# Performance work log

Measured on AMD Instinct MI355X. Metric: run time of the kernel, lower is better.

The kernel has to match this reference:

```python
import jax, jax.numpy as jnp
import numpy as np
from jax import lax

B, T, E, H, VC, VP = 128, 512, 256, 512, 64, 128


def _uniform(key, shape, bound):
    return jax.random.uniform(key, shape, minval=-bound, maxval=bound, dtype=jnp.float32)


def setup_inputs() -> dict:
    key = jax.random.key(0)
    ks = jax.random.split(key, 12)
    src = jax.random.randint(ks[0], (B, T), 0, VC)
    src_lengths = jax.random.randint(ks[1], (B,), 1, T + 1)
    # embedding table, padding_idx=0 row zeroed (as nn.Embedding does)
    emb_table = jax.random.normal(ks[2], (VC, E), dtype=jnp.float32)
    emb_table = emb_table.at[0].set(0.0)
    # layer 0: W_xh Linear(E->H, bias), W_hh Linear(H->H, no bias)
    bE, bH = 1.0 / np.sqrt(E), 1.0 / np.sqrt(H)
    W_xh0 = _uniform(ks[3], (E, H), bE)
    b_xh0 = _uniform(ks[4], (H,), bE)
    W_hh0 = _uniform(ks[5], (H, H), bH)
    # layer 1: input is hidden of layer 0
    W_xh1 = _uniform(ks[6], (H, H), bH)
    b_xh1 = _uniform(ks[7], (H,), bH)
    W_hh1 = _uniform(ks[8], (H, H), bH)
    # output projection Linear(H -> VP)
    fc_w = _uniform(ks[9], (H, VP), bH)
    fc_b = _uniform(ks[10], (VP,), bH)
    return {
        "src": src, "src_lengths": src_lengths, "emb_table": emb_table,
        "W_xh0": W_xh0, "b_xh0": b_xh0, "W_hh0": W_hh0,
        "W_xh1": W_xh1, "b_xh1": b_xh1, "W_hh1": W_hh1,
        "fc_w": fc_w, "fc_b": fc_b,
    }


def reference(src, src_lengths, emb_table, W_xh0, b_xh0, W_hh0,
              W_xh1, b_xh1, W_hh1, fc_w, fc_b):
    batch, seq_len = src.shape
    emb = emb_table[src]  # (B, T, E); dropout p=0 -> identity (eval)
    mask = jnp.arange(seq_len)[None, :] < src_lengths[:, None]  # (B, T) bool

    xs = jnp.transpose(emb, (1, 0, 2))          # (T, B, E) time-major
    ms = jnp.transpose(mask)[:, :, None]        # (T, B, 1)

    def step(h, inp):
        x_t, m_t = inp
        h0, h1 = h
        h0_new = jnp.tanh(x_t @ W_xh0 + b_xh0 + h0 @ W_hh0)
        h0 = jnp.where(m_t, h0_new, h0)
        h1_new = jnp.tanh(h0 @ W_xh1 + b_xh1 + h1 @ W_hh1)
        h1 = jnp.where(m_t, h1_new, h1)
        return (h0, h1), h1

    h_init = jnp.zeros((batch, W_hh0.shape[0]), dtype=emb.dtype)
    _, ys = lax.scan(step, (h_init, h_init), (xs, ms))  # ys: (T, B, H)
    outputs = jnp.transpose(ys, (1, 0, 2))               # (B, T, H)
    logits = outputs @ fc_w + fc_b                       # (B, T, VP)
    return logits
```

## Files before the change

kernel.cpp:

```cpp
#include <hip/hip_runtime.h>
#include <hip/hip_bf16.h>

constexpr int NB = 128;
constexpr int NT = 512;
constexpr int NE = 256;
constexpr int NH = 512;
constexpr int NV = 64;
constexpr int NP = 128;

constexpr int GROUPS = 8;
constexpr int MR     = 16;
constexpr int NCS    = 64;
constexpr int SLICES = 8;
constexpr int NBLK   = GROUPS * SLICES * 2;
constexpr int RING   = 16;
constexpr int FS     = 32;

typedef unsigned short u16;
typedef __attribute__((ext_vector_type(8))) short bf16x8v;
typedef __attribute__((ext_vector_type(4))) float f32x4v;
typedef __attribute__((ext_vector_type(4))) unsigned u32x4;

__device__ __forceinline__ u16 f2bf(float x) {
  unsigned u = __builtin_bit_cast(unsigned, x);
  return (u16)((u + 0x7fffu + ((u >> 16) & 1u)) >> 16);
}

__device__ __forceinline__ void ld4_sc1(const void* p0, const void* p1,
                                        const void* p2, const void* p3,
                                        u32x4& a, u32x4& b, u32x4& c, u32x4& d) {
  asm volatile("global_load_dwordx4 %0, %4, off sc1\n\t"
               "global_load_dwordx4 %1, %5, off sc1\n\t"
               "global_load_dwordx4 %2, %6, off sc1\n\t"
               "global_load_dwordx4 %3, %7, off sc1\n\t"
               "s_waitcnt vmcnt(0)"
               : "=&v"(a), "=&v"(b), "=&v"(c), "=&v"(d)
               : "v"(p0), "v"(p1), "v"(p2), "v"(p3) : "memory");
}
__device__ __forceinline__ void ld8_sc1(const void* p0, const void* p1,
                                        const void* p2, const void* p3,
                                        const void* p4, const void* p5,
                                        const void* p6, const void* p7,
                                        u32x4& a, u32x4& b, u32x4& c, u32x4& d,
                                        u32x4& e, u32x4& f, u32x4& g, u32x4& h) {
  asm volatile("global_load_dwordx4 %0, %8, off sc1\n\t"
               "global_load_dwordx4 %1, %9, off sc1\n\t"
               "global_load_dwordx4 %2, %10, off sc1\n\t"
               "global_load_dwordx4 %3, %11, off sc1\n\t"
               "global_load_dwordx4 %4, %12, off sc1\n\t"
               "global_load_dwordx4 %5, %13, off sc1\n\t"
               "global_load_dwordx4 %6, %14, off sc1\n\t"
               "global_load_dwordx4 %7, %15, off sc1\n\t"
               "s_waitcnt vmcnt(0)"
               : "=&v"(a), "=&v"(b), "=&v"(c), "=&v"(d),
                 "=&v"(e), "=&v"(f), "=&v"(g), "=&v"(h)
               : "v"(p0), "v"(p1), "v"(p2), "v"(p3),
                 "v"(p4), "v"(p5), "v"(p6), "v"(p7) : "memory");
}
__device__ __forceinline__ void st_sc1_x4(void* p, u32x4 v) {
  asm volatile("global_store_dwordx4 %0, %1, off sc1" :: "v"(p), "v"(v) : "memory");
}

__global__ __launch_bounds__(256) void proj_kernel(
    const float* __restrict__ emb, const float* __restrict__ W_xh0,
    const float* __restrict__ b_xh0, float* __restrict__ proj) {
  int v = blockIdx.x >> 1;
  int j = ((blockIdx.x & 1) << 8) + threadIdx.x;
  float acc = b_xh0[j];
  const float* er = emb + v * NE;
  for (int e = 0; e < NE; ++e) acc += er[e] * W_xh0[e * NH + j];
  proj[v * NH + j] = acc;
}

__global__ __launch_bounds__(256) void transpose_bf16_kernel(
    const float* __restrict__ src, u16* __restrict__ dst, int R, int logC) {
  int idx = blockIdx.x * 256 + threadIdx.x;
  int C = 1 << logC;
  if (idx >= R * C) return;
  int r = idx >> logC;
  int c = idx & (C - 1);
  dst[c * R + r] = f2bf(src[idx]);
}

__global__ void zero_flags_kernel(int* flags) {
  int i = blockIdx.x * 256 + threadIdx.x;
  if (i < 2 * 64 * FS) flags[i] = 0;
}

__device__ __forceinline__ bf16x8v frag_A(const u16* __restrict__ buf,
                                          int kt, int lane) {
  return *(const bf16x8v*)(buf + (kt << 9) + (((lane ^ kt) & 63) << 3));
}

__device__ __forceinline__ void publish_slice(const u16* __restrict__ rep,
                                              u16* __restrict__ gpanel,
                                              int sl, int tid) {
  if (tid < 128) {
    int ktl = tid >> 6, slot = tid & 63;
    int ktp = sl * 2 + ktl;
    int v = (slot ^ ktp) & 63;
    int row = v & 15, koct = (v >> 4) & 3;
    int lcol = ktl * 32 + koct * 8;
    st_sc1_x4(gpanel + ktp * 512 + slot * 8,
              *(const u32x4*)(rep + row * 64 + lcol));
  }
}

__global__ __launch_bounds__(256, 1) void rnn_persist(
    const int* __restrict__ src, const int* __restrict__ lens,
    const float* __restrict__ proj,
    const u16* __restrict__ Wt_hh0,
    const u16* __restrict__ Wt_xh1,
    const u16* __restrict__ Wt_hh1,
    const float* __restrict__ b_xh1,
    u16* __restrict__ h0f,
    u16* __restrict__ h1f,
    int* __restrict__ flags)
{
  __shared__ struct {
    union {
      struct { __attribute__((aligned(16))) u16 a0[8192];
               float pj[NV][68]; int srcv[MR][NT]; } l0;
      struct { __attribute__((aligned(16))) u16 a0[8192];
               __attribute__((aligned(16))) u16 a1[8192]; } l1;
    } u;
    __attribute__((aligned(16))) u16 rep[16][64];
  } sm;

  const int bid = blockIdx.x;
  const bool is_l1 = (bid >= 64);
  const int rb = bid & 63;
  const int g = rb & (GROUPS - 1);
  const int sl = rb >> 3;
  const int c0 = sl * NCS;
  const int r0 = g * MR;

  const int tid = threadIdx.x;
  const int lane = tid & 63, wave = tid >> 6;
  const int lq = lane >> 4, lr = lane & 15;
  const int lcol = wave * 16 + lr;

  int* flag0 = flags;
  int* flag1 = flags + 64 * FS;
  int* myflag = (is_l1 ? flag1 : flag0) + rb * FS;

  int ln[4];
#pragma unroll
  for (int i = 0; i < 4; ++i) ln[i] = lens[r0 + lq * 4 + i];
  u16 oreg[4] = {0, 0, 0, 0};

  if (!is_l1) {
    bf16x8v w0[16];
    {
      const u16* wp = Wt_hh0 + (size_t)(c0 + lcol) * NH + lq * 8;
#pragma unroll
      for (int kt = 0; kt < 16; ++kt) w0[kt] = *(const bf16x8v*)(wp + kt * 32);
    }
#pragma unroll
    for (int it = 0; it < 4; ++it) {
      int c = it * 256 + tid;
      int v = c >> 4, j4 = (c & 15) * 4;
      *(float4*)&sm.u.l0.pj[v][j4] = *(const float4*)&proj[v * NH + c0 + j4];
    }
#pragma unroll
    for (int it = 0; it < 8; ++it)
      ((int4*)sm.u.l0.srcv)[it * 256 + tid] =
          ((const int4*)(src + (size_t)r0 * NT))[it * 256 + tid];
    __syncthreads();

    for (int s = 0; s < NT; ++s) {
      f32x4v acc = {0.f, 0.f, 0.f, 0.f};
      if (s > 0) {
        if (tid < 8) {
          const int* fp = flag0 + ((tid * 8) | g) * FS;
          while (__hip_atomic_load(fp, __ATOMIC_RELAXED,
                                   __HIP_MEMORY_SCOPE_AGENT) < s) {}
        } else if (tid < 16 && s - 14 > 0) {
          const int* fp = flag1 + (((tid - 8) * 8) | g) * FS;
          while (__hip_atomic_load(fp, __ATOMIC_RELAXED,
                                   __HIP_MEMORY_SCOPE_AGENT) < s - 14) {}
        }
        if (tid < 64) __builtin_amdgcn_fence(__ATOMIC_ACQUIRE, "agent");
        __syncthreads();
        {
          const u16* gp = h0f + ((size_t)((s - 1) & (RING - 1)) * GROUPS + g) * 8192;
          u32x4 a, b, c, d;
          ld4_sc1(gp + (tid + 0) * 8, gp + (tid + 256) * 8,
                  gp + (tid + 512) * 8, gp + (tid + 768) * 8, a, b, c, d);
          *(u32x4*)(sm.u.l0.a0 + (tid + 0) * 8) = a;
          *(u32x4*)(sm.u.l0.a0 + (tid + 256) * 8) = b;
          *(u32x4*)(sm.u.l0.a0 + (tid + 512) * 8) = c;
          *(u32x4*)(sm.u.l0.a0 + (tid + 768) * 8) = d;
        }
        __syncthreads();
#pragma unroll
        for (int kt = 0; kt < 16; ++kt)
          acc = __builtin_amdgcn_mfma_f32_16x16x32_bf16(
              frag_A(sm.u.l0.a0, kt, lane), w0[kt], acc, 0, 0, 0);
      }
#pragma unroll
      for (int i = 0; i < 4; ++i) {
        int row = lq * 4 + i;
        float pre = acc[i] + sm.u.l0.pj[sm.u.l0.srcv[row][s]][lcol];
        oreg[i] = (s < ln[i]) ? f2bf(tanhf(pre)) : oreg[i];
        sm.rep[row][lcol] = oreg[i];
      }
      __syncthreads();
      publish_slice(&sm.rep[0][0],
                    h0f + ((size_t)(s & (RING - 1)) * GROUPS + g) * 8192, sl, tid);
      asm volatile("s_waitcnt vmcnt(0)" ::: "memory");
      __syncthreads();
      if (tid == 0)
        __hip_atomic_store(myflag, s + 1, __ATOMIC_RELAXED,
                           __HIP_MEMORY_SCOPE_AGENT);
    }
  } else {
    bf16x8v wx[16], wh[16];
    {
      const u16* wpx = Wt_xh1 + (size_t)(c0 + lcol) * NH + lq * 8;
      const u16* wph = Wt_hh1 + (size_t)(c0 + lcol) * NH + lq * 8;
#pragma unroll
      for (int kt = 0; kt < 16; ++kt) {
        wx[kt] = *(const bf16x8v*)(wpx + kt * 32);
        wh[kt] = *(const bf16x8v*)(wph + kt * 32);
      }
    }
    const float bcol = b_xh1[c0 + lcol];
    __syncthreads();

    for (int t = 0; t < NT; ++t) {
      if (tid < 8) {
        if (t > 0) {
          const int* fp = flag1 + ((tid * 8) | g) * FS;
          while (__hip_atomic_load(fp, __ATOMIC_RELAXED,
                                   __HIP_MEMORY_SCOPE_AGENT) < t) {}
        }
      } else if (tid < 16) {
        const int* fp = flag0 + (((tid - 8) * 8) | g) * FS;
        while (__hip_atomic_load(fp, __ATOMIC_RELAXED,
                                 __HIP_MEMORY_SCOPE_AGENT) < t + 1) {}
      }
      if (tid < 64) __builtin_amdgcn_fence(__ATOMIC_ACQUIRE, "agent");
      __syncthreads();
      {
        const u16* g0 = h0f + ((size_t)(t & (RING - 1)) * GROUPS + g) * 8192;
        if (t > 0) {
          const u16* g1 = h1f + ((size_t)(t - 1) * GROUPS + g) * 8192;
          u32x4 a, b, c, d, e, f, h, k;
          ld8_sc1(g0 + (tid + 0) * 8, g0 + (tid + 256) * 8,
                  g0 + (tid + 512) * 8, g0 + (tid + 768) * 8,
                  g1 + (tid + 0) * 8, g1 + (tid + 256) * 8,
                  g1 + (tid + 512) * 8, g1 + (tid + 768) * 8,
                  a, b, c, d, e, f, h, k);
          *(u32x4*)(sm.u.l1.a0 + (tid + 0) * 8) = a;
          *(u32x4*)(sm.u.l1.a0 + (tid + 256) * 8) = b;
          *(u32x4*)(sm.u.l1.a0 + (tid + 512) * 8) = c;
          *(u32x4*)(sm.u.l1.a0 + (tid + 768) * 8) = d;
          *(u32x4*)(sm.u.l1.a1 + (tid + 0) * 8) = e;
          *(u32x4*)(sm.u.l1.a1 + (tid + 256) * 8) = f;
          *(u32x4*)(sm.u.l1.a1 + (tid + 512) * 8) = h;
          *(u32x4*)(sm.u.l1.a1 + (tid + 768) * 8) = k;
        } else {
          u32x4 a, b, c, d;
          ld4_sc1(g0 + (tid + 0) * 8, g0 + (tid + 256) * 8,
                  g0 + (tid + 512) * 8, g0 + (tid + 768) * 8, a, b, c, d);
          *(u32x4*)(sm.u.l1.a0 + (tid + 0) * 8) = a;
          *(u32x4*)(sm.u.l1.a0 + (tid + 256) * 8) = b;
          *(u32x4*)(sm.u.l1.a0 + (tid + 512) * 8) = c;
          *(u32x4*)(sm.u.l1.a0 + (tid + 768) * 8) = d;
        }
      }
      __syncthreads();

      f32x4v accx = {0.f, 0.f, 0.f, 0.f}, acch = {0.f, 0.f, 0.f, 0.f};
#pragma unroll
      for (int kt = 0; kt < 16; ++kt)
        accx = __builtin_amdgcn_mfma_f32_16x16x32_bf16(
            frag_A(sm.u.l1.a0, kt, lane), wx[kt], accx, 0, 0, 0);
      if (t > 0) {
#pragma unroll
        for (int kt = 0; kt < 16; ++kt)
          acch = __builtin_amdgcn_mfma_f32_16x16x32_bf16(
              frag_A(sm.u.l1.a1, kt, lane), wh[kt], acch, 0, 0, 0);
      }
#pragma unroll
      for (int i = 0; i < 4; ++i) {
        int row = lq * 4 + i;
        float pre = accx[i] + acch[i] + bcol;
        oreg[i] = (t < ln[i]) ? f2bf(tanhf(pre)) : oreg[i];
        sm.rep[row][lcol] = oreg[i];
      }
      __syncthreads();
      publish_slice(&sm.rep[0][0],
                    h1f + ((size_t)t * GROUPS + g) * 8192, sl, tid);
      asm volatile("s_waitcnt vmcnt(0)" ::: "memory");
      __syncthreads();
      if (tid == 0)
        __hip_atomic_store(myflag, t + 1, __ATOMIC_RELAXED,
                           __HIP_MEMORY_SCOPE_AGENT);
    }
  }
}

__global__ __launch_bounds__(256) void out_gemm(
    const u16* __restrict__ h1f, const u16* __restrict__ fc_wT,
    const float* __restrict__ fc_b, float* __restrict__ out)
{
  const int t = blockIdx.x;
  const int tid = threadIdx.x, lane = tid & 63, wave = tid >> 6;
  const int lq = lane >> 4, lr = lane & 15;
  const int m0 = wave * 32;
  f32x4v acc[2][8];
#pragma unroll
  for (int a = 0; a < 2; ++a)
#pragma unroll
    for (int b = 0; b < 8; ++b) acc[a][b] = (f32x4v){0.f, 0.f, 0.f, 0.f};

  const u16* p0 = h1f + ((size_t)t * GROUPS + wave * 2) * 8192;
  const u16* p1 = p0 + 8192;
#pragma unroll 2
  for (int kt = 0; kt < 16; ++kt) {
    bf16x8v a0 = *(const bf16x8v*)(p0 + kt * 512 + (((lane ^ kt) & 63) << 3));
    bf16x8v a1 = *(const bf16x8v*)(p1 + kt * 512 + (((lane ^ kt) & 63) << 3));
    int kb = kt * 32 + lq * 8;
#pragma unroll
    for (int ni = 0; ni < 8; ++ni) {
      bf16x8v bb = *(const bf16x8v*)(fc_wT + (size_t)(ni * 16 + lr) * NH + kb);
      acc[0][ni] = __builtin_amdgcn_mfma_f32_16x16x32_bf16(a0, bb, acc[0][ni], 0, 0, 0);
      acc[1][ni] = __builtin_amdgcn_mfma_f32_16x16x32_bf16(a1, bb, acc[1][ni], 0, 0, 0);
    }
  }
#pragma unroll
  for (int mi = 0; mi < 2; ++mi)
#pragma unroll
    for (int ni = 0; ni < 8; ++ni)
#pragma unroll
      for (int i = 0; i < 4; ++i) {
        int b_ = m0 + mi * 16 + lq * 4 + i;
        int p = ni * 16 + lr;
        out[((size_t)b_ * NT + t) * NP + p] = acc[mi][ni][i] + fc_b[p];
      }
}

extern "C" void kernel_launch(void* const* d_in, const int* in_sizes, int n_in,
                              void* d_out, int out_size, void* d_ws, size_t ws_size,
                              hipStream_t stream) {
  const int*   src   = (const int*)  d_in[0];
  const int*   lens  = (const int*)  d_in[1];
  const float* emb   = (const float*)d_in[2];
  const float* W_xh0 = (const float*)d_in[3];
  const float* b_xh0 = (const float*)d_in[4];
  const float* W_hh0 = (const float*)d_in[5];
  const float* W_xh1 = (const float*)d_in[6];
  const float* b_xh1 = (const float*)d_in[7];
  const float* W_hh1 = (const float*)d_in[8];
  const float* fc_w  = (const float*)d_in[9];
  const float* fc_b  = (const float*)d_in[10];
  float* out = (float*)d_out;

  char* ws = (char*)d_ws;
  auto alloc = [&](size_t bytes) { char* p = ws; ws += (bytes + 255) & ~size_t(255); return p; };
  float* proj   = (float*)alloc(NV * NH * 4);
  u16* Wt_hh0   = (u16*)  alloc(NH * NH * 2);
  u16* Wt_xh1   = (u16*)  alloc(NH * NH * 2);
  u16* Wt_hh1   = (u16*)  alloc(NH * NH * 2);
  u16* fc_wT    = (u16*)  alloc(NP * NH * 2);
  u16* h0f      = (u16*)  alloc((size_t)RING * GROUPS * 8192 * 2);
  u16* h1f      = (u16*)  alloc((size_t)NT * GROUPS * 8192 * 2);
  int* flags    = (int*)  alloc(2 * 64 * FS * 4);

  proj_kernel<<<NV * 2, 256, 0, stream>>>(emb, W_xh0, b_xh0, proj);
  transpose_bf16_kernel<<<(NH * NH + 255) / 256, 256, 0, stream>>>(W_hh0, Wt_hh0, NH, 9);
  transpose_bf16_kernel<<<(NH * NH + 255) / 256, 256, 0, stream>>>(W_xh1, Wt_xh1, NH, 9);
  transpose_bf16_kernel<<<(NH * NH + 255) / 256, 256, 0, stream>>>(W_hh1, Wt_hh1, NH, 9);
  transpose_bf16_kernel<<<(NH * NP + 255) / 256, 256, 0, stream>>>(fc_w, fc_wT, NH, 7);
  zero_flags_kernel<<<(2 * 64 * FS + 255) / 256, 256, 0, stream>>>(flags);

  {
    void* kargs[] = { (void*)&src, (void*)&lens, (void*)&proj, (void*)&Wt_hh0,
                      (void*)&Wt_xh1, (void*)&Wt_hh1, (void*)&b_xh1,
                      (void*)&h0f, (void*)&h1f, (void*)&flags };
    hipError_t e = hipLaunchCooperativeKernel((void*)rnn_persist, dim3(NBLK), dim3(256),
                                              kargs, 0, stream);
    if (e != hipSuccess) {
      rnn_persist<<<NBLK, 256, 0, stream>>>(src, lens, proj, Wt_hh0, Wt_xh1,
                                            Wt_hh1, b_xh1, h0f, h1f, flags);
    }
  }

  out_gemm<<<NT, 256, 0, stream>>>(h1f, fc_wT, fc_b, out);
}
```

Measured before the change: 1.547 ms.

## Overlap flag publish with peer-flag polling across waves and drop a barrier

```diff
diff --git a/kernel.cpp b/kernel.cpp
--- a/kernel.cpp
+++ b/kernel.cpp
@@ -92,17 +92,19 @@
   return *(const bf16x8v*)(buf + (kt << 9) + (((lane ^ kt) & 63) << 3));
 }
 
-__device__ __forceinline__ void publish_slice(const u16* __restrict__ rep,
-                                              u16* __restrict__ gpanel,
-                                              int sl, int tid) {
-  if (tid < 128) {
-    int ktl = tid >> 6, slot = tid & 63;
+__device__ __forceinline__ void publish_w0(const u16* __restrict__ rep,
+                                           u16* __restrict__ gpanel,
+                                           int sl, int lane) {
+#pragma unroll
+  for (int hh = 0; hh < 2; ++hh) {
+    int c = hh * 64 + lane;
+    int ktl = c >> 6, slot = c & 63;
     int ktp = sl * 2 + ktl;
     int v = (slot ^ ktp) & 63;
     int row = v & 15, koct = (v >> 4) & 3;
-    int lcol = ktl * 32 + koct * 8;
+    int lc = ktl * 32 + koct * 8;
     st_sc1_x4(gpanel + ktp * 512 + slot * 8,
-              *(const u32x4*)(rep + row * 64 + lcol));
+              *(const u32x4*)(rep + row * 64 + lc));
   }
 }
 
@@ -171,15 +173,6 @@
     for (int s = 0; s < NT; ++s) {
       f32x4v acc = {0.f, 0.f, 0.f, 0.f};
       if (s > 0) {
-        if (tid < 8) {
-          const int* fp = flag0 + ((tid * 8) | g) * FS;
-          while (__hip_atomic_load(fp, __ATOMIC_RELAXED,
-                                   __HIP_MEMORY_SCOPE_AGENT) < s) {}
-        } else if (tid < 16 && s - 14 > 0) {
-          const int* fp = flag1 + (((tid - 8) * 8) | g) * FS;
-          while (__hip_atomic_load(fp, __ATOMIC_RELAXED,
-                                   __HIP_MEMORY_SCOPE_AGENT) < s - 14) {}
-        }
         if (tid < 64) __builtin_amdgcn_fence(__ATOMIC_ACQUIRE, "agent");
         __syncthreads();
         {
@@ -206,13 +199,28 @@
         sm.rep[row][lcol] = oreg[i];
       }
       __syncthreads();
-      publish_slice(&sm.rep[0][0],
-                    h0f + ((size_t)(s & (RING - 1)) * GROUPS + g) * 8192, sl, tid);
-      asm volatile("s_waitcnt vmcnt(0)" ::: "memory");
-      __syncthreads();
-      if (tid == 0)
-        __hip_atomic_store(myflag, s + 1, __ATOMIC_RELAXED,
-                           __HIP_MEMORY_SCOPE_AGENT);
+      if (wave == 0) {
+        publish_w0(&sm.rep[0][0],
+                   h0f + ((size_t)(s & (RING - 1)) * GROUPS + g) * 8192, sl, lane);
+        asm volatile("s_waitcnt vmcnt(0)" ::: "memory");
+        if (lane == 0)
+          __hip_atomic_store(myflag, s + 1, __ATOMIC_RELAXED,
+                             __HIP_MEMORY_SCOPE_AGENT);
+      } else if (wave == 2) {
+        if (s + 1 < NT && lane < 8 && lane != sl) {
+          const int* fp = flag0 + ((lane << 3) | g) * FS;
+          while (__hip_atomic_load(fp, __ATOMIC_RELAXED,
+                                   __HIP_MEMORY_SCOPE_AGENT) < s + 1) {}
+        }
+      } else if (wave == 3) {
+        int need = s + 1 - 14;
+        if (s + 1 < NT && lane < 8 && need > 0) {
+          const int* fp = flag1 + ((lane << 3) | g) * FS;
+          while (__hip_atomic_load(fp, __ATOMIC_RELAXED,
+                                   __HIP_MEMORY_SCOPE_AGENT) < need) {}
+        }
+      }
+      __syncthreads();
     }
   } else {
     bf16x8v wx[16], wh[16];
@@ -227,19 +235,14 @@
     }
     const float bcol = b_xh1[c0 + lcol];
     __syncthreads();
+    if (tid < 8) {
+      const int* fp = flag0 + ((tid << 3) | g) * FS;
+      while (__hip_atomic_load(fp, __ATOMIC_RELAXED,
+                               __HIP_MEMORY_SCOPE_AGENT) < 1) {}
+    }
+    __syncthreads();
 
     for (int t = 0; t < NT; ++t) {
-      if (tid < 8) {
-        if (t > 0) {
-          const int* fp = flag1 + ((tid * 8) | g) * FS;
-          while (__hip_atomic_load(fp, __ATOMIC_RELAXED,
-                                   __HIP_MEMORY_SCOPE_AGENT) < t) {}
-        }
-      } else if (tid < 16) {
-        const int* fp = flag0 + (((tid - 8) * 8) | g) * FS;
-        while (__hip_atomic_load(fp, __ATOMIC_RELAXED,
-                                 __HIP_MEMORY_SCOPE_AGENT) < t + 1) {}
-      }
       if (tid < 64) __builtin_amdgcn_fence(__ATOMIC_ACQUIRE, "agent");
       __syncthreads();
       {
@@ -291,13 +294,27 @@
         sm.rep[row][lcol] = oreg[i];
       }
       __syncthreads();
-      publish_slice(&sm.rep[0][0],
-                    h1f + ((size_t)t * GROUPS + g) * 8192, sl, tid);
-      asm volatile("s_waitcnt vmcnt(0)" ::: "memory");
-      __syncthreads();
-      if (tid == 0)
-        __hip_atomic_store(myflag, t + 1, __ATOMIC_RELAXED,
-                           __HIP_MEMORY_SCOPE_AGENT);
+      if (wave == 0) {
+        publish_w0(&sm.rep[0][0],
+                   h1f + ((size_t)t * GROUPS + g) * 8192, sl, lane);
+        asm volatile("s_waitcnt vmcnt(0)" ::: "memory");
+        if (lane == 0)
+          __hip_atomic_store(myflag, t + 1, __ATOMIC_RELAXED,
+                             __HIP_MEMORY_SCOPE_AGENT);
+      } else if (wave == 2) {
+        if (t + 1 < NT && lane < 8 && lane != sl) {
+          const int* fp = flag1 + ((lane << 3) | g) * FS;
+          while (__hip_atomic_load(fp, __ATOMIC_RELAXED,
+                                   __HIP_MEMORY_SCOPE_AGENT) < t + 1) {}
+        }
+      } else if (wave == 3) {
+        if (t + 1 < NT && lane < 8) {
+          const int* fp = flag0 + ((lane << 3) | g) * FS;
+          while (__hip_atomic_load(fp, __ATOMIC_RELAXED,
+                                   __HIP_MEMORY_SCOPE_AGENT) < t + 2) {}
+        }
+      }
+      __syncthreads();
     }
   }
 }
```

New measurement: 1.697 ms. 1.1x slower.

## Repartition persistent RNN onto fewer, wider blocks with 512 threads

Applied to the files above, without the earlier changes.

```diff
diff --git a/kernel.cpp b/kernel.cpp
--- a/kernel.cpp
+++ b/kernel.cpp
@@ -10,9 +10,11 @@
 
 constexpr int GROUPS = 8;
 constexpr int MR     = 16;
-constexpr int NCS    = 64;
-constexpr int SLICES = 8;
-constexpr int NBLK   = GROUPS * SLICES * 2;
+constexpr int SL0    = 2;
+constexpr int SL1    = 4;
+constexpr int NBLK0  = GROUPS * SL0;
+constexpr int NBLK1  = GROUPS * SL1;
+constexpr int NBLK   = NBLK0 + NBLK1;
 constexpr int RING   = 16;
 constexpr int FS     = 32;
 
@@ -26,6 +28,13 @@
   return (u16)((u + 0x7fffu + ((u >> 16) & 1u)) >> 16);
 }
 
+__device__ __forceinline__ void ld2_sc1(const void* p0, const void* p1,
+                                        u32x4& a, u32x4& b) {
+  asm volatile("global_load_dwordx4 %0, %2, off sc1\n\t"
+               "global_load_dwordx4 %1, %3, off sc1\n\t"
+               "s_waitcnt vmcnt(0)"
+               : "=&v"(a), "=&v"(b) : "v"(p0), "v"(p1) : "memory");
+}
 __device__ __forceinline__ void ld4_sc1(const void* p0, const void* p1,
                                         const void* p2, const void* p3,
                                         u32x4& a, u32x4& b, u32x4& c, u32x4& d) {
@@ -37,26 +46,6 @@
                : "=&v"(a), "=&v"(b), "=&v"(c), "=&v"(d)
                : "v"(p0), "v"(p1), "v"(p2), "v"(p3) : "memory");
 }
-__device__ __forceinline__ void ld8_sc1(const void* p0, const void* p1,
-                                        const void* p2, const void* p3,
-                                        const void* p4, const void* p5,
-                                        const void* p6, const void* p7,
-                                        u32x4& a, u32x4& b, u32x4& c, u32x4& d,
-                                        u32x4& e, u32x4& f, u32x4& g, u32x4& h) {
-  asm volatile("global_load_dwordx4 %0, %8, off sc1\n\t"
-               "global_load_dwordx4 %1, %9, off sc1\n\t"
-               "global_load_dwordx4 %2, %10, off sc1\n\t"
-               "global_load_dwordx4 %3, %11, off sc1\n\t"
-               "global_load_dwordx4 %4, %12, off sc1\n\t"
-               "global_load_dwordx4 %5, %13, off sc1\n\t"
-               "global_load_dwordx4 %6, %14, off sc1\n\t"
-               "global_load_dwordx4 %7, %15, off sc1\n\t"
-               "s_waitcnt vmcnt(0)"
-               : "=&v"(a), "=&v"(b), "=&v"(c), "=&v"(d),
-                 "=&v"(e), "=&v"(f), "=&v"(g), "=&v"(h)
-               : "v"(p0), "v"(p1), "v"(p2), "v"(p3),
-                 "v"(p4), "v"(p5), "v"(p6), "v"(p7) : "memory");
-}
 __device__ __forceinline__ void st_sc1_x4(void* p, u32x4 v) {
   asm volatile("global_store_dwordx4 %0, %1, off sc1" :: "v"(p), "v"(v) : "memory");
 }
@@ -84,7 +73,7 @@
 
 __global__ void zero_flags_kernel(int* flags) {
   int i = blockIdx.x * 256 + threadIdx.x;
-  if (i < 2 * 64 * FS) flags[i] = 0;
+  if (i < NBLK * FS) flags[i] = 0;
 }
 
 __device__ __forceinline__ bf16x8v frag_A(const u16* __restrict__ buf,
@@ -92,21 +81,7 @@
   return *(const bf16x8v*)(buf + (kt << 9) + (((lane ^ kt) & 63) << 3));
 }
 
-__device__ __forceinline__ void publish_slice(const u16* __restrict__ rep,
-                                              u16* __restrict__ gpanel,
-                                              int sl, int tid) {
-  if (tid < 128) {
-    int ktl = tid >> 6, slot = tid & 63;
-    int ktp = sl * 2 + ktl;
-    int v = (slot ^ ktp) & 63;
-    int row = v & 15, koct = (v >> 4) & 3;
-    int lcol = ktl * 32 + koct * 8;
-    st_sc1_x4(gpanel + ktp * 512 + slot * 8,
-              *(const u32x4*)(rep + row * 64 + lcol));
-  }
-}
-
-__global__ __launch_bounds__(256, 1) void rnn_persist(
+__global__ __launch_bounds__(512, 1) void rnn_persist(
     const int* __restrict__ src, const int* __restrict__ lens,
     const float* __restrict__ proj,
     const u16* __restrict__ Wt_hh0,
@@ -120,63 +95,65 @@
   __shared__ struct {
     union {
       struct { __attribute__((aligned(16))) u16 a0[8192];
-               float pj[NV][68]; int srcv[MR][NT]; } l0;
+               float pj[NV][257];
+               int srcv[MR][NT];
+               __attribute__((aligned(16))) u16 rep[16][256]; } l0;
       struct { __attribute__((aligned(16))) u16 a0[8192];
-               __attribute__((aligned(16))) u16 a1[8192]; } l1;
+               __attribute__((aligned(16))) u16 a1[8192];
+               __attribute__((aligned(16))) u16 rep[16][128]; } l1;
     } u;
-    __attribute__((aligned(16))) u16 rep[16][64];
   } sm;
 
   const int bid = blockIdx.x;
-  const bool is_l1 = (bid >= 64);
-  const int rb = bid & 63;
+  const bool is_l1 = (bid >= NBLK0);
+  const int rb = is_l1 ? (bid - NBLK0) : bid;
   const int g = rb & (GROUPS - 1);
   const int sl = rb >> 3;
-  const int c0 = sl * NCS;
   const int r0 = g * MR;
 
   const int tid = threadIdx.x;
   const int lane = tid & 63, wave = tid >> 6;
   const int lq = lane >> 4, lr = lane & 15;
-  const int lcol = wave * 16 + lr;
 
   int* flag0 = flags;
-  int* flag1 = flags + 64 * FS;
+  int* flag1 = flags + NBLK0 * FS;
   int* myflag = (is_l1 ? flag1 : flag0) + rb * FS;
 
   int ln[4];
 #pragma unroll
   for (int i = 0; i < 4; ++i) ln[i] = lens[r0 + lq * 4 + i];
-  u16 oreg[4] = {0, 0, 0, 0};
 
   if (!is_l1) {
-    bf16x8v w0[16];
-    {
-      const u16* wp = Wt_hh0 + (size_t)(c0 + lcol) * NH + lq * 8;
-#pragma unroll
-      for (int kt = 0; kt < 16; ++kt) w0[kt] = *(const bf16x8v*)(wp + kt * 32);
-    }
-#pragma unroll
-    for (int it = 0; it < 4; ++it) {
-      int c = it * 256 + tid;
-      int v = c >> 4, j4 = (c & 15) * 4;
-      *(float4*)&sm.u.l0.pj[v][j4] = *(const float4*)&proj[v * NH + c0 + j4];
-    }
-#pragma unroll
-    for (int it = 0; it < 8; ++it)
-      ((int4*)sm.u.l0.srcv)[it * 256 + tid] =
-          ((const int4*)(src + (size_t)r0 * NT))[it * 256 + tid];
+    const int c0 = sl * 256;
+    bf16x8v w0[2][16];
+#pragma unroll
+    for (int nt = 0; nt < 2; ++nt) {
+      const u16* wp = Wt_hh0 + (size_t)(c0 + wave * 32 + nt * 16 + lr) * NH + lq * 8;
+#pragma unroll
+      for (int kt = 0; kt < 16; ++kt) w0[nt][kt] = *(const bf16x8v*)(wp + kt * 32);
+    }
+#pragma unroll
+    for (int it = 0; it < 32; ++it) {
+      int idx = it * 512 + tid;
+      int v = idx >> 8, c = idx & 255;
+      sm.u.l0.pj[v][c] = proj[v * NH + c0 + c];
+    }
+#pragma unroll
+    for (int it = 0; it < 4; ++it)
+      ((int4*)sm.u.l0.srcv)[it * 512 + tid] =
+          ((const int4*)(src + (size_t)r0 * NT))[it * 512 + tid];
+    u16 oreg[2][4] = {{0,0,0,0},{0,0,0,0}};
     __syncthreads();
 
     for (int s = 0; s < NT; ++s) {
-      f32x4v acc = {0.f, 0.f, 0.f, 0.f};
+      f32x4v acc0 = {0.f,0.f,0.f,0.f}, acc1 = {0.f,0.f,0.f,0.f};
       if (s > 0) {
-        if (tid < 8) {
-          const int* fp = flag0 + ((tid * 8) | g) * FS;
+        if (tid < 2) {
+          const int* fp = flag0 + ((tid << 3) | g) * FS;
           while (__hip_atomic_load(fp, __ATOMIC_RELAXED,
                                    __HIP_MEMORY_SCOPE_AGENT) < s) {}
-        } else if (tid < 16 && s - 14 > 0) {
-          const int* fp = flag1 + (((tid - 8) * 8) | g) * FS;
+        } else if (tid >= 8 && tid < 12 && s - 14 > 0) {
+          const int* fp = flag1 + (((tid - 8) << 3) | g) * FS;
           while (__hip_atomic_load(fp, __ATOMIC_RELAXED,
                                    __HIP_MEMORY_SCOPE_AGENT) < s - 14) {}
         }
@@ -184,30 +161,42 @@
         __syncthreads();
         {
           const u16* gp = h0f + ((size_t)((s - 1) & (RING - 1)) * GROUPS + g) * 8192;
-          u32x4 a, b, c, d;
-          ld4_sc1(gp + (tid + 0) * 8, gp + (tid + 256) * 8,
-                  gp + (tid + 512) * 8, gp + (tid + 768) * 8, a, b, c, d);
-          *(u32x4*)(sm.u.l0.a0 + (tid + 0) * 8) = a;
-          *(u32x4*)(sm.u.l0.a0 + (tid + 256) * 8) = b;
-          *(u32x4*)(sm.u.l0.a0 + (tid + 512) * 8) = c;
-          *(u32x4*)(sm.u.l0.a0 + (tid + 768) * 8) = d;
+          u32x4 a, b;
+          ld2_sc1(gp + (size_t)tid * 8, gp + (size_t)(tid + 512) * 8, a, b);
+          *(u32x4*)(sm.u.l0.a0 + (size_t)tid * 8) = a;
+          *(u32x4*)(sm.u.l0.a0 + (size_t)(tid + 512) * 8) = b;
         }
         __syncthreads();
 #pragma unroll
-        for (int kt = 0; kt < 16; ++kt)
-          acc = __builtin_amdgcn_mfma_f32_16x16x32_bf16(
-              frag_A(sm.u.l0.a0, kt, lane), w0[kt], acc, 0, 0, 0);
-      }
-#pragma unroll
-      for (int i = 0; i < 4; ++i) {
-        int row = lq * 4 + i;
-        float pre = acc[i] + sm.u.l0.pj[sm.u.l0.srcv[row][s]][lcol];
-        oreg[i] = (s < ln[i]) ? f2bf(tanhf(pre)) : oreg[i];
-        sm.rep[row][lcol] = oreg[i];
-      }
-      __syncthreads();
-      publish_slice(&sm.rep[0][0],
-                    h0f + ((size_t)(s & (RING - 1)) * GROUPS + g) * 8192, sl, tid);
+        for (int kt = 0; kt < 16; ++kt) {
+          bf16x8v af = frag_A(sm.u.l0.a0, kt, lane);
+          acc0 = __builtin_amdgcn_mfma_f32_16x16x32_bf16(af, w0[0][kt], acc0, 0, 0, 0);
+          acc1 = __builtin_amdgcn_mfma_f32_16x16x32_bf16(af, w0[1][kt], acc1, 0, 0, 0);
+        }
+      }
+#pragma unroll
+      for (int nt = 0; nt < 2; ++nt) {
+        f32x4v acc = nt ? acc1 : acc0;
+        int col = wave * 32 + nt * 16 + lr;
+#pragma unroll
+        for (int i = 0; i < 4; ++i) {
+          int row = lq * 4 + i;
+          float pre = acc[i] + sm.u.l0.pj[sm.u.l0.srcv[row][s]][col];
+          oreg[nt][i] = (s < ln[i]) ? f2bf(tanhf(pre)) : oreg[nt][i];
+          sm.u.l0.rep[row][col] = oreg[nt][i];
+        }
+      }
+      __syncthreads();
+      {
+        u16* gpanel = h0f + ((size_t)(s & (RING - 1)) * GROUPS + g) * 8192;
+        int ktl = tid >> 6, slot = tid & 63;
+        int ktp = sl * 8 + ktl;
+        int v = (slot ^ ktp) & 63;
+        int row = v & 15, koct = (v >> 4) & 3;
+        int lc = ktl * 32 + koct * 8;
+        st_sc1_x4(gpanel + ktp * 512 + slot * 8,
+                  *(const u32x4*)(&sm.u.l0.rep[row][lc]));
+      }
       asm volatile("s_waitcnt vmcnt(0)" ::: "memory");
       __syncthreads();
       if (tid == 0)
@@ -215,6 +204,8 @@
                            __HIP_MEMORY_SCOPE_AGENT);
     }
   } else {
+    const int c0 = sl * 128;
+    const int lcol = wave * 16 + lr;
     bf16x8v wx[16], wh[16];
     {
       const u16* wpx = Wt_xh1 + (size_t)(c0 + lcol) * NH + lq * 8;
@@ -226,17 +217,18 @@
       }
     }
     const float bcol = b_xh1[c0 + lcol];
+    u16 oreg[4] = {0, 0, 0, 0};
     __syncthreads();
 
     for (int t = 0; t < NT; ++t) {
-      if (tid < 8) {
+      if (tid < 4) {
         if (t > 0) {
-          const int* fp = flag1 + ((tid * 8) | g) * FS;
+          const int* fp = flag1 + ((tid << 3) | g) * FS;
           while (__hip_atomic_load(fp, __ATOMIC_RELAXED,
                                    __HIP_MEMORY_SCOPE_AGENT) < t) {}
         }
-      } else if (tid < 16) {
-        const int* fp = flag0 + (((tid - 8) * 8) | g) * FS;
+      } else if (tid >= 8 && tid < 10) {
+        const int* fp = flag0 + (((tid - 8) << 3) | g) * FS;
         while (__hip_atomic_load(fp, __ATOMIC_RELAXED,
                                  __HIP_MEMORY_SCOPE_AGENT) < t + 1) {}
       }
@@ -246,33 +238,24 @@
         const u16* g0 = h0f + ((size_t)(t & (RING - 1)) * GROUPS + g) * 8192;
         if (t > 0) {
           const u16* g1 = h1f + ((size_t)(t - 1) * GROUPS + g) * 8192;
-          u32x4 a, b, c, d, e, f, h, k;
-          ld8_sc1(g0 + (tid + 0) * 8, g0 + (tid + 256) * 8,
-                  g0 + (tid + 512) * 8, g0 + (tid + 768) * 8,
-                  g1 + (tid + 0) * 8, g1 + (tid + 256) * 8,
-                  g1 + (tid + 512) * 8, g1 + (tid + 768) * 8,
-                  a, b, c, d, e, f, h, k);
-          *(u32x4*)(sm.u.l1.a0 + (tid + 0) * 8) = a;
-          *(u32x4*)(sm.u.l1.a0 + (tid + 256) * 8) = b;
-          *(u32x4*)(sm.u.l1.a0 + (tid + 512) * 8) = c;
-          *(u32x4*)(sm.u.l1.a0 + (tid + 768) * 8) = d;
-          *(u32x4*)(sm.u.l1.a1 + (tid + 0) * 8) = e;
-          *(u32x4*)(sm.u.l1.a1 + (tid + 256) * 8) = f;
-          *(u32x4*)(sm.u.l1.a1 + (tid + 512) * 8) = h;
-          *(u32x4*)(sm.u.l1.a1 + (tid + 768) * 8) = k;
+          u32x4 a, b, c, d;
+          ld4_sc1(g0 + (size_t)tid * 8, g0 + (size_t)(tid + 512) * 8,
+                  g1 + (size_t)tid * 8, g1 + (size_t)(tid + 512) * 8,
+                  a, b, c, d);
+          *(u32x4*)(sm.u.l1.a0 + (size_t)tid * 8) = a;
+          *(u32x4*)(sm.u.l1.a0 + (size_t)(tid + 512) * 8) = b;
+          *(u32x4*)(sm.u.l1.a1 + (size_t)tid * 8) = c;
+          *(u32x4*)(sm.u.l1.a1 + (size_t)(tid + 512) * 8) = d;
         } else {
-          u32x4 a, b, c, d;
-          ld4_sc1(g0 + (tid + 0) * 8, g0 + (tid + 256) * 8,
-                  g0 + (tid + 512) * 8, g0 + (tid + 768) * 8, a, b, c, d);
-          *(u32x4*)(sm.u.l1.a0 + (tid + 0) * 8) = a;
-          *(u32x4*)(sm.u.l1.a0 + (tid + 256) * 8) = b;
-          *(u32x4*)(sm.u.l1.a0 + (tid + 512) * 8) = c;
-          *(u32x4*)(sm.u.l1.a0 + (tid + 768) * 8) = d;
-        }
-      }
-      __syncthreads();
-
-      f32x4v accx = {0.f, 0.f, 0.f, 0.f}, acch = {0.f, 0.f, 0.f, 0.f};
+          u32x4 a, b;
+          ld2_sc1(g0 + (size_t)tid * 8, g0 + (size_t)(tid + 512) * 8, a, b);
+          *(u32x4*)(sm.u.l1.a0 + (size_t)tid * 8) = a;
+          *(u32x4*)(sm.u.l1.a0 + (size_t)(tid + 512) * 8) = b;
+        }
+      }
+      __syncthreads();
+
+      f32x4v accx = {0.f,0.f,0.f,0.f}, acch = {0.f,0.f,0.f,0.f};
 #pragma unroll
       for (int kt = 0; kt < 16; ++kt)
         accx = __builtin_amdgcn_mfma_f32_16x16x32_bf16(
@@ -288,11 +271,19 @@
         int row = lq * 4 + i;
         float pre = accx[i] + acch[i] + bcol;
         oreg[i] = (t < ln[i]) ? f2bf(tanhf(pre)) : oreg[i];
-        sm.rep[row][lcol] = oreg[i];
-      }
-      __syncthreads();
-      publish_slice(&sm.rep[0][0],
-                    h1f + ((size_t)t * GROUPS + g) * 8192, sl, tid);
+        sm.u.l1.rep[row][lcol] = oreg[i];
+      }
+      __syncthreads();
+      if (tid < 256) {
+        u16* gpanel = h1f + ((size_t)t * GROUPS + g) * 8192;
+        int ktl = tid >> 6, slot = tid & 63;
+        int ktp = sl * 4 + ktl;
+        int v = (slot ^ ktp) & 63;
+        int row = v & 15, koct = (v >> 4) & 3;
+        int lc = ktl * 32 + koct * 8;
+        st_sc1_x4(gpanel + ktp * 512 + slot * 8,
+                  *(const u32x4*)(&sm.u.l1.rep[row][lc]));
+      }
       asm volatile("s_waitcnt vmcnt(0)" ::: "memory");
       __syncthreads();
       if (tid == 0)
@@ -367,23 +358,23 @@
   u16* fc_wT    = (u16*)  alloc(NP * NH * 2);
   u16* h0f      = (u16*)  alloc((size_t)RING * GROUPS * 8192 * 2);
   u16* h1f      = (u16*)  alloc((size_t)NT * GROUPS * 8192 * 2);
-  int* flags    = (int*)  alloc(2 * 64 * FS * 4);
+  int* flags    = (int*)  alloc(NBLK * FS * 4);
 
   proj_kernel<<<NV * 2, 256, 0, stream>>>(emb, W_xh0, b_xh0, proj);
   transpose_bf16_kernel<<<(NH * NH + 255) / 256, 256, 0, stream>>>(W_hh0, Wt_hh0, NH, 9);
   transpose_bf16_kernel<<<(NH * NH + 255) / 256, 256, 0, stream>>>(W_xh1, Wt_xh1, NH, 9);
   transpose_bf16_kernel<<<(NH * NH + 255) / 256, 256, 0, stream>>>(W_hh1, Wt_hh1, NH, 9);
   transpose_bf16_kernel<<<(NH * NP + 255) / 256, 256, 0, stream>>>(fc_w, fc_wT, NH, 7);
-  zero_flags_kernel<<<(2 * 64 * FS + 255) / 256, 256, 0, stream>>>(flags);
+  zero_flags_kernel<<<(NBLK * FS + 255) / 256, 256, 0, stream>>>(flags);
 
   {
     void* kargs[] = { (void*)&src, (void*)&lens, (void*)&proj, (void*)&Wt_hh0,
                       (void*)&Wt_xh1, (void*)&Wt_hh1, (void*)&b_xh1,
                       (void*)&h0f, (void*)&h1f, (void*)&flags };
-    hipError_t e = hipLaunchCooperativeKernel((void*)rnn_persist, dim3(NBLK), dim3(256),
+    hipError_t e = hipLaunchCooperativeKernel((void*)rnn_persist, dim3(NBLK), dim3(512),
                                               kargs, 0, stream);
     if (e != hipSuccess) {
-      rnn_persist<<<NBLK, 256, 0, stream>>>(src, lens, proj, Wt_hh0, Wt_xh1,
+      rnn_persist<<<NBLK, 512, 0, stream>>>(src, lens, proj, Wt_hh0, Wt_xh1,
                                             Wt_hh1, b_xh1, h0f, h1f, flags);
     }
   }
```

After: 1.799 ms. +16.3%, slower.
